# Performance work log

Measured on AMD Instinct MI355X. Metric: run time of the kernel, lower is better.

Reference implementation:

```python
import jax, jax.numpy as jnp
import numpy as np

B, CIN, COUT, H, W, WDIM = 16, 256, 256, 64, 64, 512


def setup_inputs() -> dict:
    key = jax.random.key(0)
    ks = jax.random.split(key, 4)
    return {
        "x": jax.random.normal(ks[0], (B, CIN, H, W), dtype=jnp.float32),
        "w": jax.random.normal(ks[1], (B, WDIM), dtype=jnp.float32),
        "affine_w": jax.random.normal(ks[2], (CIN, WDIM), dtype=jnp.float32),
        "affine_b": jnp.ones((CIN,), dtype=jnp.float32),
        "weight": jax.random.normal(ks[3], (COUT, CIN, 1, 1), dtype=jnp.float32),
        "bias": jnp.zeros((COUT,), dtype=jnp.float32),
    }


def reference(x, w, affine_w, affine_b, weight, bias):
    # Affine: FullyConnectedLayer with weight_gain = 1/sqrt(w_dim), bias_init=1
    wg = 1.0 / np.sqrt(WDIM).astype(np.float32)
    styles = w @ (affine_w.T * wg) + affine_b  # [B, CIN]

    # Pre-normalize weight and styles (demodulate branch)
    wk = weight[:, :, 0, 0]  # [COUT, CIN] (1x1 kernel)
    wk = wk * jax.lax.rsqrt(jnp.mean(jnp.square(weight), axis=(1, 2, 3)))[:, None]
    s = styles * jax.lax.rsqrt(jnp.mean(jnp.square(styles)))  # [B, CIN]

    # Per-sample modulated weights: [B, COUT, CIN]
    wb = wk[None, :, :] * s[:, None, :]
    dcoef = jax.lax.rsqrt(jnp.sum(jnp.square(wb), axis=2) + 1e-8)  # [B, COUT]
    wb = wb * dcoef[:, :, None]

    # Grouped 1x1 conv == batched GEMM over spatial positions
    y = jnp.einsum('bihw,boi->bohw', x, wb) + bias[None, :, None, None]

    # Bilinear upsample x2 (align_corners=False == half-pixel, jax default)
    y = jax.image.resize(y, (B, COUT, 2 * H, 2 * W), method='bilinear')
    return y
```

## Files before the change

kernel.cpp:

```cpp
#include <hip/hip_runtime.h>
#include <hip/hip_bf16.h>

#define B_   16
#define CIN  256
#define COUT 256
#define HH   64
#define WW   64
#define WDIM 512
#define OH   128
#define OW   128

#define LDK 264
#define TPX 192
#define PXP 196
#define MCH 32

typedef __attribute__((ext_vector_type(8))) short short8;
typedef __attribute__((ext_vector_type(4))) float f32x4;

__device__ __forceinline__ unsigned short f2bf(float f) {
    __hip_bfloat16 h = __float2bfloat16(f);
    return *reinterpret_cast<unsigned short*>(&h);
}


__global__ __launch_bounds__(256) void k_styles(const float* __restrict__ w,
                                                const float* __restrict__ aw,
                                                const float* __restrict__ ab,
                                                float* __restrict__ ws) {
    int b = blockIdx.x, i = threadIdx.x;
    const float4* wr = (const float4*)(w + b * WDIM);
    const float4* ar = (const float4*)(aw + (size_t)i * WDIM);
    float acc = 0.f;
    #pragma unroll 4
    for (int k = 0; k < WDIM / 4; ++k) {
        float4 wv = wr[k], av = ar[k];
        acc += wv.x * av.x + wv.y * av.y + wv.z * av.z + wv.w * av.w;
    }
    const float wg = 0.04419417382415922f;
    float st = acc * wg + ab[i];
    ws[64 + b * CIN + i] = st;
    __shared__ float sred[256];
    sred[i] = st * st;
    __syncthreads();
    for (int s = 128; s > 0; s >>= 1) {
        if (i < s) sred[i] += sred[i + s];
        __syncthreads();
    }
    if (i == 0) ws[b] = sred[0];
}

__global__ __launch_bounds__(64) void k_wb(const float* __restrict__ weight,
                                           const float* __restrict__ ws,
                                           unsigned short* __restrict__ wb) {
    int o = blockIdx.x, b = blockIdx.y, l = threadIdx.x;
    float tot = 0.f;
    #pragma unroll
    for (int j = 0; j < B_; ++j) tot += ws[j];
    float srs = rsqrtf(tot / (float)(B_ * CIN));
    float4 wk = *(const float4*)(weight + (size_t)o * CIN + l * 4);
    float ss = wk.x * wk.x + wk.y * wk.y + wk.z * wk.z + wk.w * wk.w;
    #pragma unroll
    for (int off = 32; off; off >>= 1) ss += __shfl_xor(ss, off);
    float wkn = rsqrtf(ss / (float)CIN);
    float4 st = *(const float4*)(ws + 64 + b * CIN + l * 4);
    float4 t;
    t.x = wk.x * wkn * st.x * srs;
    t.y = wk.y * wkn * st.y * srs;
    t.z = wk.z * wkn * st.z * srs;
    t.w = wk.w * wkn * st.w * srs;
    float s2 = t.x * t.x + t.y * t.y + t.z * t.z + t.w * t.w;
    #pragma unroll
    for (int off = 32; off; off >>= 1) s2 += __shfl_xor(s2, off);
    float dcoef = rsqrtf(s2 + 1e-8f);
    ushort4 pk;
    pk.x = f2bf(t.x * dcoef);
    pk.y = f2bf(t.y * dcoef);
    pk.z = f2bf(t.z * dcoef);
    pk.w = f2bf(t.w * dcoef);
    *(ushort4*)(wb + ((size_t)b * COUT + o) * CIN + l * 4) = pk;
}

__global__ __launch_bounds__(512) void k_main(const float* __restrict__ x,
                                              const float* __restrict__ bias,
                                              const unsigned short* __restrict__ wb,
                                              float* __restrict__ out) {
    __shared__ __align__(16) unsigned short xt[TPX * LDK];
    __shared__ __align__(16) float ylds[MCH * PXP];
    const int t = blockIdx.x;
    const int b = blockIdx.y;
    const int tid = threadIdx.x;
    const int lane = tid & 63, wv = tid >> 6;
    const int rowbase = 2 * t - 1;

    {
        const int g = tid & 15;
        const int k8 = tid >> 4;
        const float* xb = x + (size_t)b * CIN * HH * WW;
        #pragma unroll
        for (int i = 0; i < 3; ++i) {
            int p = g * 12 + i * 4;
            int lr = p >> 6, c = p & 63;
            int grow = rowbase + lr;
            grow = min(max(grow, 0), HH - 1);
            int gp = grow * WW + c;
            float4 v[8];
            #pragma unroll
            for (int kk = 0; kk < 8; ++kk)
                v[kk] = *(const float4*)(xb + (size_t)(k8 * 8 + kk) * (HH * WW) + gp);
            #pragma unroll
            for (int j = 0; j < 4; ++j) {
                union { short8 s; unsigned short u[8]; } pk;
                #pragma unroll
                for (int kk = 0; kk < 8; ++kk) {
                    float f = (j == 0) ? v[kk].x : (j == 1) ? v[kk].y : (j == 2) ? v[kk].z : v[kk].w;
                    pk.u[kk] = f2bf(f);
                }
                *reinterpret_cast<short8*>(&xt[(p + j) * LDK + k8 * 8]) = pk.s;
            }
        }
    }
    __syncthreads();

    const int wm = wv & 1, wn = wv >> 1;
    const int n0 = wn * 48;
    const int hi = lane >> 4, lo = lane & 15;
    const unsigned short* wbp = wb + (size_t)b * COUT * CIN;

    const int ostart = (t == 0) ? 0 : (4 * t - 1);
    const int oend = (t == 31) ? 128 : (4 * t + 3);
    const int nrows = oend - ostart;
    const int iters = 2 * nrows;

    for (int mc = 0; mc < COUT / MCH; ++mc) {
        const int m0 = mc * MCH + wm * 16;
        f32x4 acc0 = {0.f, 0.f, 0.f, 0.f};
        f32x4 acc1 = {0.f, 0.f, 0.f, 0.f};
        f32x4 acc2 = {0.f, 0.f, 0.f, 0.f};
        #pragma unroll
        for (int ks = 0; ks < 8; ++ks) {
            const int k0 = ks * 32;
            short8 a = *(const short8*)(wbp + (size_t)(m0 + lo) * CIN + k0 + hi * 8);
            short8 b0 = *(const short8*)&xt[(n0 + lo) * LDK + k0 + hi * 8];
            short8 b1 = *(const short8*)&xt[(n0 + 16 + lo) * LDK + k0 + hi * 8];
            short8 b2 = *(const short8*)&xt[(n0 + 32 + lo) * LDK + k0 + hi * 8];
            acc0 = __builtin_amdgcn_mfma_f32_16x16x32_bf16(a, b0, acc0, 0, 0, 0);
            acc1 = __builtin_amdgcn_mfma_f32_16x16x32_bf16(a, b1, acc1, 0, 0, 0);
            acc2 = __builtin_amdgcn_mfma_f32_16x16x32_bf16(a, b2, acc2, 0, 0, 0);
        }
        const int mloc = wm * 16 + hi * 4;
        #pragma unroll
        for (int j = 0; j < 4; ++j) {
            float bs = bias[mc * MCH + mloc + j];
            ylds[(mloc + j) * PXP + n0 + lo]      = acc0[j] + bs;
            ylds[(mloc + j) * PXP + n0 + 16 + lo] = acc1[j] + bs;
            ylds[(mloc + j) * PXP + n0 + 32 + lo] = acc2[j] + bs;
        }
        __syncthreads();

        for (int it = 0; it < iters; ++it) {
            int f = it * 512 + tid;
            int q = f & 31;
            int rest = f >> 5;
            int ch = rest & 31;
            int ori = rest >> 5;
            int o = ostart + ori;
            int yr0 = (o - 1) >> 1;
            int lr0 = min(max(yr0, 0), HH - 1) - rowbase;
            int lr1 = min(max(yr0 + 1, 0), HH - 1) - rowbase;
            float wr0 = (o & 1) ? 0.75f : 0.25f;
            float wr1 = 1.f - wr0;
            int cA = max(2 * q - 1, 0), cB = 2 * q;
            int cC = min(2 * q + 1, WW - 1), cD = min(2 * q + 2, WW - 1);
            const float* Y = &ylds[ch * PXP];
            float rA = wr0 * Y[lr0 * 64 + cA] + wr1 * Y[lr1 * 64 + cA];
            float rB = wr0 * Y[lr0 * 64 + cB] + wr1 * Y[lr1 * 64 + cB];
            float rC = wr0 * Y[lr0 * 64 + cC] + wr1 * Y[lr1 * 64 + cC];
            float rD = wr0 * Y[lr0 * 64 + cD] + wr1 * Y[lr1 * 64 + cD];
            float4 ov;
            ov.x = 0.25f * rA + 0.75f * rB;
            ov.y = 0.75f * rB + 0.25f * rC;
            ov.z = 0.25f * rB + 0.75f * rC;
            ov.w = 0.75f * rC + 0.25f * rD;
            float* op = out + ((((size_t)b * COUT + mc * MCH + ch) * OH + o) * OW + q * 4);
            *(float4*)op = ov;
        }
        __syncthreads();
    }
}

extern "C" void kernel_launch(void* const* d_in, const int* in_sizes, int n_in,
                              void* d_out, int out_size, void* d_ws, size_t ws_size,
                              hipStream_t stream) {
    (void)in_sizes; (void)n_in; (void)out_size; (void)ws_size;
    const float* x      = (const float*)d_in[0];
    const float* w      = (const float*)d_in[1];
    const float* aw     = (const float*)d_in[2];
    const float* ab     = (const float*)d_in[3];
    const float* weight = (const float*)d_in[4];
    const float* bias   = (const float*)d_in[5];
    float* out = (float*)d_out;
    float* wsf = (float*)d_ws;
    unsigned short* wb = (unsigned short*)((char*)d_ws + 32768);

    hipLaunchKernelGGL(k_styles, dim3(16), dim3(256), 0, stream, w, aw, ab, wsf);
    hipLaunchKernelGGL(k_wb, dim3(COUT, B_), dim3(64), 0, stream, weight, wsf, wb);
    hipLaunchKernelGGL(k_main, dim3(32, B_), dim3(512), 0, stream, x, bias, wb, out);
}
```

Baseline: 126.1 us.

## Shrink main kernel tile to two input rows and store intermediate in bf16 LDS

Each block now handles one input row pair (128 pixels) instead of a three-row tile, giving 64 row blocks per sample and a launch bound requesting four blocks per CU. The post-GEMM tile is kept in LDS as bf16 rather than fp32, cutting shared memory so more blocks fit. The cost is more redundant halo loading of x and more recomputed GEMM rows, plus extra rounding of the intermediate before interpolation.

```diff
diff --git a/kernel.cpp b/kernel.cpp
--- a/kernel.cpp
+++ b/kernel.cpp
@@ -10,10 +10,10 @@
 #define OH   128
 #define OW   128
 
-#define LDK 264
-#define TPX 192
-#define PXP 196
-#define MCH 32
+#define PX   128
+#define LDK  264
+#define YLP  136
+#define MCH  32
 
 typedef __attribute__((ext_vector_type(8))) short short8;
 typedef __attribute__((ext_vector_type(4))) float f32x4;
@@ -21,6 +21,10 @@
 __device__ __forceinline__ unsigned short f2bf(float f) {
     __hip_bfloat16 h = __float2bfloat16(f);
     return *reinterpret_cast<unsigned short*>(&h);
+}
+__device__ __forceinline__ float bf2f(unsigned short u) {
+    unsigned int t = ((unsigned int)u) << 16;
+    return *reinterpret_cast<float*>(&t);
 }
 
 
@@ -81,54 +85,53 @@
     *(ushort4*)(wb + ((size_t)b * COUT + o) * CIN + l * 4) = pk;
 }
 
-__global__ __launch_bounds__(512) void k_main(const float* __restrict__ x,
-                                              const float* __restrict__ bias,
-                                              const unsigned short* __restrict__ wb,
-                                              float* __restrict__ out) {
-    __shared__ __align__(16) unsigned short xt[TPX * LDK];
-    __shared__ __align__(16) float ylds[MCH * PXP];
-    const int t = blockIdx.x;
+__global__ __launch_bounds__(512, 4) void k_main(const float* __restrict__ x,
+                                                 const float* __restrict__ bias,
+                                                 const unsigned short* __restrict__ wb,
+                                                 float* __restrict__ out) {
+    __shared__ __align__(16) unsigned short xt[PX * LDK];
+    __shared__ __align__(16) unsigned short ylds[MCH * YLP];
+    const int r = blockIdx.x;
     const int b = blockIdx.y;
     const int tid = threadIdx.x;
-    const int lane = tid & 63, wv = tid >> 6;
-    const int rowbase = 2 * t - 1;
+    const int lane = tid & 63;
 
     {
-        const int g = tid & 15;
-        const int k8 = tid >> 4;
-        const float* xb = x + (size_t)b * CIN * HH * WW;
+        const int g = tid & 31;
+        const int kk = tid >> 5;
+        const int row = g >> 4;
+        const int col4 = (g & 15) * 4;
+        const int grow = min(r + row, HH - 1);
+        const float* xp = x + (size_t)b * CIN * HH * WW + grow * WW + col4;
+        const int px0 = g * 4;
         #pragma unroll
-        for (int i = 0; i < 3; ++i) {
-            int p = g * 12 + i * 4;
-            int lr = p >> 6, c = p & 63;
-            int grow = rowbase + lr;
-            grow = min(max(grow, 0), HH - 1);
-            int gp = grow * WW + c;
+        for (int grp = 0; grp < 2; ++grp) {
             float4 v[8];
             #pragma unroll
-            for (int kk = 0; kk < 8; ++kk)
-                v[kk] = *(const float4*)(xb + (size_t)(k8 * 8 + kk) * (HH * WW) + gp);
+            for (int c = 0; c < 8; ++c)
+                v[c] = *(const float4*)(xp + (size_t)(kk * 16 + grp * 8 + c) * (HH * WW));
             #pragma unroll
             for (int j = 0; j < 4; ++j) {
                 union { short8 s; unsigned short u[8]; } pk;
                 #pragma unroll
-                for (int kk = 0; kk < 8; ++kk) {
-                    float f = (j == 0) ? v[kk].x : (j == 1) ? v[kk].y : (j == 2) ? v[kk].z : v[kk].w;
-                    pk.u[kk] = f2bf(f);
+                for (int c = 0; c < 8; ++c) {
+                    float f = (j == 0) ? v[c].x : (j == 1) ? v[c].y : (j == 2) ? v[c].z : v[c].w;
+                    pk.u[c] = f2bf(f);
                 }
-                *reinterpret_cast<short8*>(&xt[(p + j) * LDK + k8 * 8]) = pk.s;
+                *reinterpret_cast<short8*>(&xt[(px0 + j) * LDK + kk * 16 + grp * 8]) = pk.s;
             }
         }
     }
     __syncthreads();
 
+    const int wv = tid >> 6;
     const int wm = wv & 1, wn = wv >> 1;
-    const int n0 = wn * 48;
+    const int n0 = wn * 32;
     const int hi = lane >> 4, lo = lane & 15;
     const unsigned short* wbp = wb + (size_t)b * COUT * CIN;
 
-    const int ostart = (t == 0) ? 0 : (4 * t - 1);
-    const int oend = (t == 31) ? 128 : (4 * t + 3);
+    const int ostart = (r == 0) ? 0 : (2 * r + 1);
+    const int oend = (r == HH - 1) ? OH : (2 * r + 3);
     const int nrows = oend - ostart;
     const int iters = 2 * nrows;
 
@@ -136,47 +139,42 @@
         const int m0 = mc * MCH + wm * 16;
         f32x4 acc0 = {0.f, 0.f, 0.f, 0.f};
         f32x4 acc1 = {0.f, 0.f, 0.f, 0.f};
-        f32x4 acc2 = {0.f, 0.f, 0.f, 0.f};
         #pragma unroll
         for (int ks = 0; ks < 8; ++ks) {
             const int k0 = ks * 32;
-            short8 a = *(const short8*)(wbp + (size_t)(m0 + lo) * CIN + k0 + hi * 8);
+            short8 a  = *(const short8*)(wbp + (size_t)(m0 + lo) * CIN + k0 + hi * 8);
             short8 b0 = *(const short8*)&xt[(n0 + lo) * LDK + k0 + hi * 8];
             short8 b1 = *(const short8*)&xt[(n0 + 16 + lo) * LDK + k0 + hi * 8];
-            short8 b2 = *(const short8*)&xt[(n0 + 32 + lo) * LDK + k0 + hi * 8];
             acc0 = __builtin_amdgcn_mfma_f32_16x16x32_bf16(a, b0, acc0, 0, 0, 0);
             acc1 = __builtin_amdgcn_mfma_f32_16x16x32_bf16(a, b1, acc1, 0, 0, 0);
-            acc2 = __builtin_amdgcn_mfma_f32_16x16x32_bf16(a, b2, acc2, 0, 0, 0);
         }
         const int mloc = wm * 16 + hi * 4;
         #pragma unroll
         for (int j = 0; j < 4; ++j) {
             float bs = bias[mc * MCH + mloc + j];
-            ylds[(mloc + j) * PXP + n0 + lo]      = acc0[j] + bs;
-            ylds[(mloc + j) * PXP + n0 + 16 + lo] = acc1[j] + bs;
-            ylds[(mloc + j) * PXP + n0 + 32 + lo] = acc2[j] + bs;
+            ylds[(mloc + j) * YLP + n0 + lo]      = f2bf(acc0[j] + bs);
+            ylds[(mloc + j) * YLP + n0 + 16 + lo] = f2bf(acc1[j] + bs);
         }
         __syncthreads();
 
         for (int it = 0; it < iters; ++it) {
             int f = it * 512 + tid;
             int q = f & 31;
-            int rest = f >> 5;
-            int ch = rest & 31;
-            int ori = rest >> 5;
+            int ch = (f >> 5) & 31;
+            int ori = f >> 10;
             int o = ostart + ori;
             int yr0 = (o - 1) >> 1;
-            int lr0 = min(max(yr0, 0), HH - 1) - rowbase;
-            int lr1 = min(max(yr0 + 1, 0), HH - 1) - rowbase;
+            int lr0 = min(max(yr0, 0), HH - 1) - r;
+            int lr1 = min(yr0 + 1, HH - 1) - r;
             float wr0 = (o & 1) ? 0.75f : 0.25f;
             float wr1 = 1.f - wr0;
             int cA = max(2 * q - 1, 0), cB = 2 * q;
             int cC = min(2 * q + 1, WW - 1), cD = min(2 * q + 2, WW - 1);
-            const float* Y = &ylds[ch * PXP];
-            float rA = wr0 * Y[lr0 * 64 + cA] + wr1 * Y[lr1 * 64 + cA];
-            float rB = wr0 * Y[lr0 * 64 + cB] + wr1 * Y[lr1 * 64 + cB];
-            float rC = wr0 * Y[lr0 * 64 + cC] + wr1 * Y[lr1 * 64 + cC];
-            float rD = wr0 * Y[lr0 * 64 + cD] + wr1 * Y[lr1 * 64 + cD];
+            const unsigned short* Y = &ylds[ch * YLP];
+            float rA = wr0 * bf2f(Y[lr0 * 64 + cA]) + wr1 * bf2f(Y[lr1 * 64 + cA]);
+            float rB = wr0 * bf2f(Y[lr0 * 64 + cB]) + wr1 * bf2f(Y[lr1 * 64 + cB]);
+            float rC = wr0 * bf2f(Y[lr0 * 64 + cC]) + wr1 * bf2f(Y[lr1 * 64 + cC]);
+            float rD = wr0 * bf2f(Y[lr0 * 64 + cD]) + wr1 * bf2f(Y[lr1 * 64 + cD]);
             float4 ov;
             ov.x = 0.25f * rA + 0.75f * rB;
             ov.y = 0.75f * rB + 0.25f * rC;
@@ -205,5 +203,5 @@
 
     hipLaunchKernelGGL(k_styles, dim3(16), dim3(256), 0, stream, w, aw, ab, wsf);
     hipLaunchKernelGGL(k_wb, dim3(COUT, B_), dim3(64), 0, stream, weight, wsf, wb);
-    hipLaunchKernelGGL(k_main, dim3(32, B_), dim3(512), 0, stream, x, bias, wb, out);
-}
+    hipLaunchKernelGGL(k_main, dim3(HH, B_), dim3(512), 0, stream, x, bias, wb, out);
+}
```

Result: faster. 122.9 us (-2.5%).
